# Optimization experiments

Hardware: AMD Instinct MI355X
Metric: run time of the kernel (lower is better)

Reference implementation:

```python
import jax, jax.numpy as jnp
import numpy as np

OUT = 7          # output_size
SR = 2           # sampling_ratio
SCALES = (0.25, 0.125, 0.0625, 0.03125)
K_MIN, K_MAX = 2, 5   # -log2(scales[0]), -log2(scales[-1])
CANON_SCALE, CANON_LVL, EPS = 224.0, 4.0, 1e-6


def _roi_align_level(feat, b_idx, boxes, scale):
    """ROIAlign (maskrcnn-benchmark, non-aligned) of all boxes on one level.
    feat: [B,C,H,W], b_idx: [N] int, boxes: [N,4] xyxy in image coords.
    Returns [N,C,OUT,OUT]."""
    N = boxes.shape[0]
    H, W = feat.shape[2], feat.shape[3]
    x1 = boxes[:, 0] * scale
    y1 = boxes[:, 1] * scale
    x2 = boxes[:, 2] * scale
    y2 = boxes[:, 3] * scale
    roi_w = jnp.maximum(x2 - x1, 1.0)
    roi_h = jnp.maximum(y2 - y1, 1.0)
    bin_w = roi_w / OUT
    bin_h = roi_h / OUT
    # sample positions inside each bin, in bin units: [OUT*SR]
    sub = (jnp.arange(SR, dtype=feat.dtype) + 0.5) / SR
    grid1d = (jnp.arange(OUT, dtype=feat.dtype)[:, None] + sub[None, :]).reshape(-1)
    ys = y1[:, None] + bin_h[:, None] * grid1d[None, :]   # [N, OUT*SR]
    xs = x1[:, None] + bin_w[:, None] * grid1d[None, :]   # [N, OUT*SR]
    K = OUT * SR
    Yf = jnp.broadcast_to(ys[:, :, None], (N, K, K)).reshape(N, K * K)
    Xf = jnp.broadcast_to(xs[:, None, :], (N, K, K)).reshape(N, K * K)
    valid = (Yf >= -1.0) & (Yf <= H) & (Xf >= -1.0) & (Xf <= W)
    y = jnp.clip(Yf, 0.0, H - 1)
    x = jnp.clip(Xf, 0.0, W - 1)
    y0 = jnp.floor(y).astype(jnp.int32)
    x0 = jnp.floor(x).astype(jnp.int32)
    y1i = jnp.minimum(y0 + 1, H - 1)
    x1i = jnp.minimum(x0 + 1, W - 1)
    ly = y - y0
    lx = x - x0
    hy = 1.0 - ly
    hx = 1.0 - lx
    b = b_idx[:, None]  # [N,1] broadcasts with [N,K*K]
    def g(yi, xi):
        return feat[b, :, yi, xi]  # [N, K*K, C]
    val = (g(y0, x0) * (hy * hx)[..., None]
           + g(y0, x1i) * (hy * lx)[..., None]
           + g(y1i, x0) * (ly * hx)[..., None]
           + g(y1i, x1i) * (ly * lx)[..., None])
    val = jnp.where(valid[..., None], val, 0.0)
    # [N, OUT, SR, OUT, SR, C] -> average sampling points -> [N, OUT, OUT, C]
    val = val.reshape(N, OUT, SR, OUT, SR, -1).mean(axis=(2, 4))
    return jnp.transpose(val, (0, 3, 1, 2))  # [N, C, OUT, OUT]


def _map_levels(boxes):
    # BoxList.area with TO_REMOVE = 1 (xyxy mode)
    area = (boxes[:, 2] - boxes[:, 0] + 1.0) * (boxes[:, 3] - boxes[:, 1] + 1.0)
    s = jnp.sqrt(area)
    lvl = jnp.floor(CANON_LVL + jnp.log2(s / CANON_SCALE + EPS))
    lvl = jnp.clip(lvl, K_MIN, K_MAX)
    return lvl.astype(jnp.int32) - K_MIN  # 0..3


def setup_inputs() -> dict:
    key = jax.random.key(0)
    ks = jax.random.split(key, 10)
    N = 1024
    H_img, W_img = 800.0, 1216.0
    x1 = jax.random.uniform(ks[0], (N,), minval=0.0, maxval=W_img - 64.0)
    y1 = jax.random.uniform(ks[1], (N,), minval=0.0, maxval=H_img - 64.0)
    w = jax.random.uniform(ks[2], (N,), minval=8.0, maxval=500.0)
    h = jax.random.uniform(ks[3], (N,), minval=8.0, maxval=500.0)
    x2 = jnp.minimum(x1 + w, W_img - 1.0)
    y2 = jnp.minimum(y1 + h, H_img - 1.0)
    boxes = jnp.stack([x1, y1, x2, y2], axis=1).astype(jnp.float32)
    box_batch_idx = jnp.sort(jax.random.randint(ks[4], (N,), 0, 2)).astype(jnp.int32)
    f0 = jax.random.normal(ks[5], (2, 256, 200, 304), dtype=jnp.float32)
    f1 = jax.random.normal(ks[6], (2, 256, 100, 152), dtype=jnp.float32)
    f2 = jax.random.normal(ks[7], (2, 256, 50, 76), dtype=jnp.float32)
    f3 = jax.random.normal(ks[8], (2, 256, 25, 38), dtype=jnp.float32)
    return {"f0": f0, "f1": f1, "f2": f2, "f3": f3,
            "boxes": boxes, "box_batch_idx": box_batch_idx}


def reference(f0, f1, f2, f3, boxes, box_batch_idx):
    feats = (f0, f1, f2, f3)
    levels = _map_levels(boxes)  # [N] in 0..3
    out = None
    for lvl, (feat, scale) in enumerate(zip(feats, SCALES)):
        pooled = _roi_align_level(feat, box_batch_idx, boxes, scale)
        mask = (levels == lvl)[:, None, None, None]
        part = jnp.where(mask, pooled, 0.0)
        out = part if out is None else out + part
    return out  # [N, C, OUT, OUT]
```

## Files before the change

kernel.cpp:

```cpp
#include <hip/hip_runtime.h>
#include <math.h>

#define TILE_PX 1280
#define MAXS 10

__global__ __launch_bounds__(128) void pooler_kernel(
    const float* __restrict__ f0, const float* __restrict__ f1,
    const float* __restrict__ f2, const float* __restrict__ f3,
    const float* __restrict__ boxes, const int* __restrict__ bidx,
    float* __restrict__ out, int N)
{
  __shared__ __align__(16) float tile[2][TILE_PX * 2];
  const int tid  = threadIdx.x;
  const int wave = tid >> 6, lane = tid & 63;
  const int n    = blockIdx.y;
  if (n >= N) return;

  const float bx1 = boxes[4*n+0], by1 = boxes[4*n+1];
  const float bx2 = boxes[4*n+2], by2 = boxes[4*n+3];
  const float area = (bx2 - bx1 + 1.0f) * (by2 - by1 + 1.0f);
  const float s    = sqrtf(area);
  int lvl = (int)floorf(4.0f + log2f(s / 224.0f + 1e-6f));
  lvl = lvl < 2 ? 2 : (lvl > 5 ? 5 : lvl);
  const int li = lvl - 2;

  int H, W; const float* feat; float scale;
  switch (li) {
    case 0:  feat = f0; H = 200; W = 304; scale = 0.25f;    break;
    case 1:  feat = f1; H = 100; W = 152; scale = 0.125f;   break;
    case 2:  feat = f2; H = 50;  W = 76;  scale = 0.0625f;  break;
    default: feat = f3; H = 25;  W = 38;  scale = 0.03125f; break;
  }
  const int b = bidx[n];
  const float x1s = bx1 * scale, y1s = by1 * scale;
  const float roiw = fmaxf(bx2 * scale - x1s, 1.0f);
  const float roih = fmaxf(by2 * scale - y1s, 1.0f);
  const float binw = roiw / 7.0f, binh = roih / 7.0f;
  const float Hm1f = (float)(H - 1), Wm1f = (float)(W - 1);
  const int   Hm1  = H - 1,          Wm1  = W - 1;

  const float yA = fminf(fmaxf(y1s + binh * 0.25f, 0.0f), Hm1f);
  const float yB = fminf(fmaxf(y1s + binh * 6.75f, 0.0f), Hm1f);
  const float xA = fminf(fmaxf(x1s + binw * 0.25f, 0.0f), Wm1f);
  const float xB = fminf(fmaxf(x1s + binw * 6.75f, 0.0f), Wm1f);
  const int y_lo = (int)yA;
  const int y_hi = min((int)yB + 1, Hm1);
  const int regH = y_hi - y_lo + 1;
  const int x_lo = ((int)xA) & ~1;
  const int x_hi = min((int)xB + 1, Wm1);
  int regW = x_hi - x_lo + 1;
  regW += (regW & 1);
  int npx = regH * regW;
  if (npx > TILE_PX) npx = TILE_PX;
  const int npair = npx >> 1;

  const int bin = (lane < 49) ? lane : 0;
  const int ph = bin / 7, pw = bin - (bin / 7) * 7;
  int   rT[2], rB[2], c0[2], c1[2];
  float hy[2], ly[2], vy[2], hx[2], lx[2], vx[2];
#pragma unroll
  for (int t = 0; t < 2; ++t) {
    const float gy = (float)ph + 0.25f + 0.5f * (float)t;
    const float Yf = y1s + binh * gy;
    vy[t] = (Yf >= -1.0f && Yf <= (float)H) ? 1.0f : 0.0f;
    const float y  = fminf(fmaxf(Yf, 0.0f), Hm1f);
    const int  y0  = (int)y;
    ly[t] = y - (float)y0;  hy[t] = 1.0f - ly[t];
    rT[t] = y0 - y_lo;
    rB[t] = min(y0 + 1, Hm1) - y_lo;

    const float gx = (float)pw + 0.25f + 0.5f * (float)t;
    const float Xf = x1s + binw * gx;
    vx[t] = (Xf >= -1.0f && Xf <= (float)W) ? 1.0f : 0.0f;
    const float x  = fminf(fmaxf(Xf, 0.0f), Wm1f);
    const int  x0  = (int)x;
    lx[t] = x - (float)x0;  hx[t] = 1.0f - lx[t];
    c0[t] = x0 - x_lo;
    c1[t] = min(x0 + 1, Wm1) - x_lo;
  }
  float wgt[16]; int ads[16];
#pragma unroll
  for (int sy = 0; sy < 2; ++sy)
#pragma unroll
    for (int sx = 0; sx < 2; ++sx) {
      const int   kk   = (sy * 2 + sx) * 4;
      const float base = vy[sy] * vx[sx] * 0.25f;
      wgt[kk+0] = hy[sy] * hx[sx] * base;  ads[kk+0] = (rT[sy]*regW + c0[sx]) * 8;
      wgt[kk+1] = hy[sy] * lx[sx] * base;  ads[kk+1] = (rT[sy]*regW + c1[sx]) * 8;
      wgt[kk+2] = ly[sy] * hx[sx] * base;  ads[kk+2] = (rB[sy]*regW + c0[sx]) * 8;
      wgt[kk+3] = ly[sy] * lx[sx] * base;  ads[kk+3] = (rB[sy]*regW + c1[sx]) * 8;
    }
#pragma unroll
  for (int kk = 0; kk < 16; ++kk)
    ads[kk] = min(ads[kk], (TILE_PX * 2 - 2) * 4);

  int goff[MAXS];
#pragma unroll
  for (int s2 = 0; s2 < MAXS; ++s2) {
    const int pi = lane + (s2 << 6);
    if (pi < npair) {
      const int p = pi << 1;
      const int r = p / regW;
      goff[s2] = r * W + (p - r * regW);
    } else goff[s2] = -1;
  }

  const size_t planeHW = (size_t)H * W;
  const int    cbase   = (blockIdx.x << 5) + (wave << 4);
  const float* pA   = feat + ((size_t)(b * 256 + cbase)) * planeHW
                           + (size_t)y_lo * W + x_lo;
  float*       outp = out + ((size_t)n * 256 + cbase) * 49 + lane;
  float*       myt  = tile[wave];

  for (int cc = 0; cc < 8; ++cc) {
    const float* p0 = pA;
    const float* p1 = pA + planeHW;
    float2 va[MAXS], vb[MAXS];
#pragma unroll
    for (int s2 = 0; s2 < MAXS; ++s2)
      if (goff[s2] >= 0) {
        va[s2] = *(const float2*)(p0 + goff[s2]);
        vb[s2] = *(const float2*)(p1 + goff[s2]);
      }
#pragma unroll
    for (int s2 = 0; s2 < MAXS; ++s2)
      if (goff[s2] >= 0) {
        const float4 q = make_float4(va[s2].x, vb[s2].x, va[s2].y, vb[s2].y);
        *(float4*)&myt[(lane + (s2 << 6)) << 2] = q;
      }
    __builtin_amdgcn_wave_barrier();

    if (lane < 49) {
      float a0 = 0.0f, a1 = 0.0f;
#pragma unroll
      for (int kk = 0; kk < 16; ++kk) {
        const float2 v = *(const float2*)((const char*)myt + ads[kk]);
        a0 = fmaf(wgt[kk], v.x, a0);
        a1 = fmaf(wgt[kk], v.y, a1);
      }
      outp[0]  = a0;
      outp[49] = a1;
    }
    __builtin_amdgcn_wave_barrier();
    pA   += 2 * planeHW;
    outp += 98;
  }
}

extern "C" void kernel_launch(void* const* d_in, const int* in_sizes, int n_in,
                              void* d_out, int out_size, void* d_ws, size_t ws_size,
                              hipStream_t stream) {
  const float* f0    = (const float*)d_in[0];
  const float* f1    = (const float*)d_in[1];
  const float* f2    = (const float*)d_in[2];
  const float* f3    = (const float*)d_in[3];
  const float* boxes = (const float*)d_in[4];
  const int*   bidx  = (const int*)d_in[5];
  const int N = in_sizes[5];
  dim3 grid(8, N);
  pooler_kernel<<<grid, 128, 0, stream>>>(f0, f1, f2, f3, boxes, bidx,
                                          (float*)d_out, N);
}
```

Baseline: 318.1 us.

## Stage only sampled rows into LDS via async global_load_lds with double buffering

Instead of loading the full bounding rectangle of the ROI into registers and writing it to LDS, the kernel builds a per-wave list of only the feature rows actually touched by sample points and uses direct global-to-LDS loads (16-byte when aligned, 4-byte for the coarsest level) into two ping-pong buffers. Each iteration processes one channel, overlapping the fetch of the next plane with the bilinear accumulation of the current one. This is meant to cut redundant row traffic and register/LDS-store overhead. The cost is a serial per-thread row-list loop, capped tile size that may truncate large regions, and reliance on vmcnt waits for correctness.

After: 283.0 us. 1.12x faster.

```diff
diff --git a/kernel.cpp b/kernel.cpp
--- a/kernel.cpp
+++ b/kernel.cpp
@@ -1,8 +1,22 @@
 #include <hip/hip_runtime.h>
 #include <math.h>
 
-#define TILE_PX 1280
-#define MAXS 10
+#define TC4  288
+#define TFL  (TC4*4)
+#define MAXS 5
+
+typedef __attribute__((address_space(3))) void lds_void;
+typedef const __attribute__((address_space(1))) void g_void;
+
+__device__ __forceinline__ void dma16(const float* g, float* l) {
+  __builtin_amdgcn_global_load_lds((g_void*)g, (lds_void*)l, 16, 0, 0);
+}
+__device__ __forceinline__ void dma4(const float* g, float* l) {
+  __builtin_amdgcn_global_load_lds((g_void*)g, (lds_void*)l, 4, 0, 0);
+}
+__device__ __forceinline__ void waitvm() {
+  asm volatile("s_waitcnt vmcnt(0)" ::: "memory");
+}
 
 __global__ __launch_bounds__(128) void pooler_kernel(
     const float* __restrict__ f0, const float* __restrict__ f1,
@@ -10,7 +24,8 @@
     const float* __restrict__ boxes, const int* __restrict__ bidx,
     float* __restrict__ out, int N)
 {
-  __shared__ __align__(16) float tile[2][TILE_PX * 2];
+  __shared__ __align__(16) float tiles[2][2][TFL];
+  __shared__ int rowlist[2][32];
   const int tid  = threadIdx.x;
   const int wave = tid >> 6, lane = tid & 63;
   const int n    = blockIdx.y;
@@ -38,36 +53,70 @@
   const float binw = roiw / 7.0f, binh = roih / 7.0f;
   const float Hm1f = (float)(H - 1), Wm1f = (float)(W - 1);
   const int   Hm1  = H - 1,          Wm1  = W - 1;
-
-  const float yA = fminf(fmaxf(y1s + binh * 0.25f, 0.0f), Hm1f);
-  const float yB = fminf(fmaxf(y1s + binh * 6.75f, 0.0f), Hm1f);
+  const bool  vec  = (li != 3);
+
   const float xA = fminf(fmaxf(x1s + binw * 0.25f, 0.0f), Wm1f);
   const float xB = fminf(fmaxf(x1s + binw * 6.75f, 0.0f), Wm1f);
-  const int y_lo = (int)yA;
-  const int y_hi = min((int)yB + 1, Hm1);
-  const int regH = y_hi - y_lo + 1;
-  const int x_lo = ((int)xA) & ~1;
-  const int x_hi = min((int)xB + 1, Wm1);
-  int regW = x_hi - x_lo + 1;
-  regW += (regW & 1);
-  int npx = regH * regW;
-  if (npx > TILE_PX) npx = TILE_PX;
-  const int npair = npx >> 1;
+  const int x_lo  = (int)xA;
+  const int x_lo4 = x_lo & ~3;
+  const int x_hi  = min((int)xB + 1, Wm1);
+  int row4 = (x_hi - x_lo4 + 4) >> 2;
+  row4 |= 1;
+  const int regW    = x_hi - x_lo + 1;
+  const int colbase = vec ? x_lo4 : x_lo;
+  const int rs_f    = vec ? (row4 << 2) : regW;
+  const int rs_c    = vec ? row4 : regW;
+  const size_t planeHW = (size_t)H * W;
 
   const int bin = (lane < 49) ? lane : 0;
   const int ph = bin / 7, pw = bin - (bin / 7) * 7;
-  int   rT[2], rB[2], c0[2], c1[2];
+  const int iA = 2 * ph, iB = iA + 1;
+  int sT[2], sB[2];
+  int R;
+  {
+    int cnt = -1, prev = -1;
+    for (int i = 0; i < 14; ++i) {
+      const float g  = (float)(i >> 1) + 0.25f + 0.5f * (float)(i & 1);
+      const float Yf = y1s + binh * g;
+      const float y  = fminf(fmaxf(Yf, 0.0f), Hm1f);
+      const int  y0  = (int)y;
+      const int  y1i = min(y0 + 1, Hm1);
+      if (y0 > prev)  { ++cnt; prev = y0;  rowlist[wave][cnt] = y0; }
+      const int s0q = cnt - (prev - y0);
+      if (y1i > prev) { ++cnt; prev = y1i; rowlist[wave][cnt] = y1i; }
+      const int s1q = cnt - (prev - y1i);
+      if (i == iA) { sT[0] = s0q; sB[0] = s1q; }
+      if (i == iB) { sT[1] = s0q; sB[1] = s1q; }
+    }
+    R = cnt + 1;
+  }
+
+  int goffA[MAXS];
+  {
+    int cntc = R * rs_c;
+    const int cap = vec ? TC4 : (MAXS * 64);
+    if (cntc > cap) cntc = cap;
+    for (int i2 = 0; i2 < MAXS; ++i2) {
+      const int u = lane + (i2 << 6);
+      if (u < cntc) {
+        const int k = u / rs_c, c = u - k * rs_c;
+        const int row = rowlist[wave][k];
+        int off = row * W + colbase + (vec ? (c << 2) : c);
+        off = min(off, (int)planeHW - (vec ? 4 : 1));
+        goffA[i2] = off;
+      } else goffA[i2] = -1;
+    }
+  }
+
   float hy[2], ly[2], vy[2], hx[2], lx[2], vx[2];
+  int   c0[2], c1[2];
 #pragma unroll
   for (int t = 0; t < 2; ++t) {
     const float gy = (float)ph + 0.25f + 0.5f * (float)t;
     const float Yf = y1s + binh * gy;
     vy[t] = (Yf >= -1.0f && Yf <= (float)H) ? 1.0f : 0.0f;
     const float y  = fminf(fmaxf(Yf, 0.0f), Hm1f);
-    const int  y0  = (int)y;
-    ly[t] = y - (float)y0;  hy[t] = 1.0f - ly[t];
-    rT[t] = y0 - y_lo;
-    rB[t] = min(y0 + 1, Hm1) - y_lo;
+    ly[t] = y - (float)((int)y);  hy[t] = 1.0f - ly[t];
 
     const float gx = (float)pw + 0.25f + 0.5f * (float)t;
     const float Xf = x1s + binw * gx;
@@ -75,75 +124,63 @@
     const float x  = fminf(fmaxf(Xf, 0.0f), Wm1f);
     const int  x0  = (int)x;
     lx[t] = x - (float)x0;  hx[t] = 1.0f - lx[t];
-    c0[t] = x0 - x_lo;
-    c1[t] = min(x0 + 1, Wm1) - x_lo;
+    c0[t] = x0 - colbase;
+    c1[t] = min(x0 + 1, Wm1) - colbase;
   }
   float wgt[16]; int ads[16];
 #pragma unroll
-  for (int sy = 0; sy < 2; ++sy)
+  for (int sy = 0; sy < 2; ++sy) {
+    const int rT = sT[sy] * rs_f, rB = sB[sy] * rs_f;
 #pragma unroll
     for (int sx = 0; sx < 2; ++sx) {
       const int   kk   = (sy * 2 + sx) * 4;
       const float base = vy[sy] * vx[sx] * 0.25f;
-      wgt[kk+0] = hy[sy] * hx[sx] * base;  ads[kk+0] = (rT[sy]*regW + c0[sx]) * 8;
-      wgt[kk+1] = hy[sy] * lx[sx] * base;  ads[kk+1] = (rT[sy]*regW + c1[sx]) * 8;
-      wgt[kk+2] = ly[sy] * hx[sx] * base;  ads[kk+2] = (rB[sy]*regW + c0[sx]) * 8;
-      wgt[kk+3] = ly[sy] * lx[sx] * base;  ads[kk+3] = (rB[sy]*regW + c1[sx]) * 8;
-    }
+      wgt[kk+0] = hy[sy] * hx[sx] * base;  ads[kk+0] = rT + c0[sx];
+      wgt[kk+1] = hy[sy] * lx[sx] * base;  ads[kk+1] = rT + c1[sx];
+      wgt[kk+2] = ly[sy] * hx[sx] * base;  ads[kk+2] = rB + c0[sx];
+      wgt[kk+3] = ly[sy] * lx[sx] * base;  ads[kk+3] = rB + c1[sx];
+    }
+  }
 #pragma unroll
   for (int kk = 0; kk < 16; ++kk)
-    ads[kk] = min(ads[kk], (TILE_PX * 2 - 2) * 4);
-
-  int goff[MAXS];
-#pragma unroll
-  for (int s2 = 0; s2 < MAXS; ++s2) {
-    const int pi = lane + (s2 << 6);
-    if (pi < npair) {
-      const int p = pi << 1;
-      const int r = p / regW;
-      goff[s2] = r * W + (p - r * regW);
-    } else goff[s2] = -1;
-  }
-
-  const size_t planeHW = (size_t)H * W;
-  const int    cbase   = (blockIdx.x << 5) + (wave << 4);
-  const float* pA   = feat + ((size_t)(b * 256 + cbase)) * planeHW
-                           + (size_t)y_lo * W + x_lo;
-  float*       outp = out + ((size_t)n * 256 + cbase) * 49 + lane;
-  float*       myt  = tile[wave];
-
-  for (int cc = 0; cc < 8; ++cc) {
-    const float* p0 = pA;
-    const float* p1 = pA + planeHW;
-    float2 va[MAXS], vb[MAXS];
-#pragma unroll
-    for (int s2 = 0; s2 < MAXS; ++s2)
-      if (goff[s2] >= 0) {
-        va[s2] = *(const float2*)(p0 + goff[s2]);
-        vb[s2] = *(const float2*)(p1 + goff[s2]);
-      }
-#pragma unroll
-    for (int s2 = 0; s2 < MAXS; ++s2)
-      if (goff[s2] >= 0) {
-        const float4 q = make_float4(va[s2].x, vb[s2].x, va[s2].y, vb[s2].y);
-        *(float4*)&myt[(lane + (s2 << 6)) << 2] = q;
-      }
-    __builtin_amdgcn_wave_barrier();
-
+    ads[kk] = min(max(ads[kk], 0), TFL - 1);
+
+  const int    cbase = (blockIdx.x << 5) + (wave << 4);
+  const float* pl    = feat + ((size_t)(b * 256 + cbase)) * planeHW;
+  float*       op    = out + ((size_t)n * 256 + cbase) * 49 + lane;
+  float* const tb0   = &tiles[wave][0][0];
+  float* const tb1   = &tiles[wave][1][0];
+
+  auto stage = [&](const float* plane, float* tb) {
+    if (vec) {
+#pragma unroll
+      for (int i2 = 0; i2 < MAXS; ++i2)
+        if (goffA[i2] >= 0) dma16(plane + goffA[i2], tb + (i2 << 8));
+    } else {
+#pragma unroll
+      for (int i2 = 0; i2 < MAXS; ++i2)
+        if (goffA[i2] >= 0) dma4(plane + goffA[i2], tb + (i2 << 6));
+    }
+  };
+  auto compute = [&](const float* tb, float* o) {
     if (lane < 49) {
-      float a0 = 0.0f, a1 = 0.0f;
-#pragma unroll
-      for (int kk = 0; kk < 16; ++kk) {
-        const float2 v = *(const float2*)((const char*)myt + ads[kk]);
-        a0 = fmaf(wgt[kk], v.x, a0);
-        a1 = fmaf(wgt[kk], v.y, a1);
-      }
-      outp[0]  = a0;
-      outp[49] = a1;
-    }
-    __builtin_amdgcn_wave_barrier();
-    pA   += 2 * planeHW;
-    outp += 98;
+      float acc = 0.0f;
+#pragma unroll
+      for (int kk = 0; kk < 16; ++kk)
+        acc = fmaf(wgt[kk], tb[ads[kk]], acc);
+      *o = acc;
+    }
+  };
+
+  stage(pl, tb0);
+  for (int cp = 0; cp < 8; ++cp) {
+    waitvm();
+    stage(pl + planeHW, tb1);
+    compute(tb0, op);  op += 49;
+    waitvm();
+    if (cp < 7) stage(pl + 2 * planeHW, tb0);
+    compute(tb1, op);  op += 49;
+    pl += 2 * planeHW;
   }
 }
 
```
